# Optimization experiments

Measured on AMD Instinct MI355X. Metric: run time of the kernel, lower is better.

## Reference

```python
import jax, jax.numpy as jnp
import numpy as np

NUM_HEADS = 16
ROPE_BASE = 50.0


def _apply_rope(x):
    # x: [b, s, h, d]; torchtune-style rotary embedding with base=ROPE_BASE
    b, s, h, d = x.shape
    inv_freq = 1.0 / (ROPE_BASE ** (jnp.arange(0, d, 2, dtype=jnp.float32) / d))  # [d/2]
    angles = jnp.arange(s, dtype=jnp.float32)[:, None] * inv_freq[None, :]         # [s, d/2]
    cos = jnp.cos(angles)[None, :, None, :]  # [1, s, 1, d/2]
    sin = jnp.sin(angles)[None, :, None, :]
    xr = x.reshape(b, s, h, d // 2, 2)
    x0, x1 = xr[..., 0], xr[..., 1]
    out = jnp.stack([x0 * cos - x1 * sin, x1 * cos + x0 * sin], axis=-1)
    return out.reshape(b, s, h, d).astype(x.dtype)


def setup_inputs() -> dict:
    key = jax.random.key(0)
    k1, k2, k3 = jax.random.split(key, 3)
    B, S, D = 2, 2048, 1024
    x = jax.random.normal(k1, (B, S, D), dtype=jnp.float32)
    w_qkv = jax.random.normal(k2, (3 * D, D), dtype=jnp.float32) * (D ** -0.5)
    w_out = jax.random.normal(k3, (D, D), dtype=jnp.float32) * (D ** -0.5)
    b_out = jnp.zeros((D,), dtype=jnp.float32)
    return {"x": x, "w_qkv": w_qkv, "w_out": w_out, "b_out": b_out}


def reference(x, w_qkv, w_out, b_out):
    B, S, D = x.shape
    H = NUM_HEADS
    dk = D // H

    qkv = x @ w_qkv.T                       # [b, s, 3D]
    q, k, v = jnp.split(qkv, 3, axis=-1)
    q = q.reshape(B, S, H, dk)
    k = k.reshape(B, S, H, dk)
    q = _apply_rope(q)
    k = _apply_rope(k)
    q = q.transpose(0, 2, 1, 3)             # [b, h, s, d]
    k = k.transpose(0, 2, 1, 3)
    v = v.reshape(B, S, H, dk).transpose(0, 2, 1, 3)

    scale = 1.0 / jnp.sqrt(jnp.asarray(dk, dtype=x.dtype))
    scores = jnp.einsum('bhsd,bhtd->bhst', q, k) * scale  # [b, h, s, s]
    # additive diagonal mask: -inf on the diagonal (blocks self-attention)
    eye = jnp.eye(S, dtype=bool)
    scores = jnp.where(eye[None, None], -jnp.inf, scores)
    attn = jax.nn.softmax(scores, axis=-1)
    out = jnp.einsum('bhst,bhtd->bhsd', attn, v)          # [b, h, s, d]
    out = out.transpose(0, 2, 1, 3).reshape(B, S, D)
    return out @ w_out.T + b_out
```

## Files before the change

### kernel.cpp

```cpp
#include <hip/hip_runtime.h>
#include <hip/hip_bf16.h>
#include <math.h>
#include <type_traits>

#define D_MODEL 1024
#define NHEADS  16
#define DK      64
#define SEQ     2048
#define BATCH   2
#define QTILE   256

typedef __attribute__((ext_vector_type(8)))  short  short8;
typedef __attribute__((ext_vector_type(8)))  unsigned short ushort8;
typedef __attribute__((ext_vector_type(4)))  float  floatx4;
typedef __attribute__((ext_vector_type(16))) float  floatx16;

template <int N> using IC = std::integral_constant<int, N>;

__device__ __forceinline__ unsigned short f2bf(float f) {
    union { float f; unsigned int u; } v; v.f = f;
    unsigned int u = v.u;
    return (unsigned short)((u + 0x7FFFu + ((u >> 16) & 1u)) >> 16);
}
__device__ __forceinline__ float bf2f(unsigned short u) {
    union { unsigned int u; float f; } v; v.u = ((unsigned int)u) << 16;
    return v.f;
}
__device__ __forceinline__ unsigned int fau(float f) {
    union { float f; unsigned int u; } v; v.f = f; return v.u;
}

__device__ __forceinline__ void gload_lds16(const unsigned short* g, unsigned short* l) {
    __builtin_amdgcn_global_load_lds((__attribute__((address_space(1))) const void*)g,
                                     (__attribute__((address_space(3))) void*)l,
                                     16, 0, 0);
}

#define X8 ((BATCH * SEQ * D_MODEL) / 8)
#define W8 ((3 * D_MODEL * D_MODEL) / 8)
#define O8 ((D_MODEL * D_MODEL) / 8)
__global__ __launch_bounds__(256) void pack_all(const float* __restrict__ x,
                                                const float* __restrict__ wq,
                                                const float* __restrict__ wo,
                                                unsigned short* __restrict__ xb,
                                                unsigned short* __restrict__ wqb,
                                                unsigned short* __restrict__ wob) {
    const int t = blockIdx.x * blockDim.x + threadIdx.x;
    const float* src; unsigned short* dst; int idx;
    if (t < X8)           { src = x;  dst = xb;  idx = t; }
    else if (t < X8 + W8) { src = wq; dst = wqb; idx = t - X8; }
    else if (t < X8 + W8 + O8) { src = wo; dst = wob; idx = t - X8 - W8; }
    else return;
    const float4 a = ((const float4*)src)[2 * idx];
    const float4 b = ((const float4*)src)[2 * idx + 1];
    short8 o;
    o[0] = (short)f2bf(a.x); o[1] = (short)f2bf(a.y);
    o[2] = (short)f2bf(a.z); o[3] = (short)f2bf(a.w);
    o[4] = (short)f2bf(b.x); o[5] = (short)f2bf(b.y);
    o[6] = (short)f2bf(b.z); o[7] = (short)f2bf(b.w);
    ((short8*)dst)[idx] = o;
}

#define QKV_M 4096
#define QKV_N 3072
#define QKV_K 1024
#define QKV_NT (QKV_K / 64)

__global__ __launch_bounds__(512, 2) void gemm_qkv_8ph(const unsigned short* __restrict__ A,
                                                        const unsigned short* __restrict__ B,
                                                        unsigned short* __restrict__ C) {
    __shared__ __align__(16) unsigned short As[2][256][64];
    __shared__ __align__(16) unsigned short Bs[2][256][64];

    const int tid  = threadIdx.x;
    const int w    = tid >> 6;
    const int lane = tid & 63;
    const int quad = lane >> 4;
    const int lcol = lane & 15;
    const int wr   = w >> 2;
    const int wc   = w & 3;

    const int f  = blockIdx.x;
    const int wg = (f & 7) * 24 + (f >> 3);
    const int tn = (wg % (QKV_N / 256)) * 256;
    const int tm = (wg / (QKV_N / 256)) * 256;

    const int srow8 = lane >> 3;
    const int sj    = lane & 7;

    auto stageA = [&](int buf, int kt, int mh) {
#pragma unroll
        for (int c = 0; c < 2; ++c) {
            const int r0 = mh * 64 + c * 128 + w * 8;
            const int r  = r0 + srow8;
            gload_lds16(A + (size_t)(tm + r) * QKV_K + kt * 64 + ((sj ^ (r & 7)) * 8),
                        &As[buf][r0][0]);
        }
    };
    auto stageB = [&](int buf, int kt, int nh) {
#pragma unroll
        for (int c = 0; c < 2; ++c) {
            const int rho0 = c * 64 + w * 8;
            const int r0   = (rho0 >> 5) * 64 + nh * 32 + (rho0 & 31);
            const int r    = r0 + srow8;
            gload_lds16(B + (size_t)(tn + r) * QKV_K + kt * 64 + ((sj ^ (r & 7)) * 8),
                        &Bs[buf][r0][0]);
        }
    };

    floatx4 acc[8][4];
#pragma unroll
    for (int i = 0; i < 8; ++i)
#pragma unroll
        for (int j = 0; j < 4; ++j) acc[i][j] = (floatx4){0.f, 0.f, 0.f, 0.f};

    auto do_phase = [&](int buf, auto vmc, auto kkc, auto mhc, auto stager) {
        constexpr int VM = decltype(vmc)::value;
        constexpr int kk = decltype(kkc)::value;
        constexpr int mh = decltype(mhc)::value;
        if constexpr (VM == 2) asm volatile("s_waitcnt vmcnt(2)" ::: "memory");
        else                   asm volatile("s_waitcnt vmcnt(4)" ::: "memory");
        __builtin_amdgcn_s_barrier();
        asm volatile("" ::: "memory");
        short8 a[4], b[4];
#pragma unroll
        for (int i = 0; i < 4; ++i) {
            const int r = wr * 128 + mh * 64 + i * 16 + lcol;
            a[i] = *(const short8*)&As[buf][r][((kk * 4 + quad) ^ (r & 7)) * 8];
        }
#pragma unroll
        for (int j = 0; j < 4; ++j) {
            const int r = wc * 64 + j * 16 + lcol;
            b[j] = *(const short8*)&Bs[buf][r][((kk * 4 + quad) ^ (r & 7)) * 8];
        }
        stager();
        __builtin_amdgcn_s_setprio(1);
#pragma unroll
        for (int i = 0; i < 4; ++i)
#pragma unroll
            for (int j = 0; j < 4; ++j)
                acc[mh * 4 + i][j] = __builtin_amdgcn_mfma_f32_16x16x32_bf16(
                    a[i], b[j], acc[mh * 4 + i][j], 0, 0, 0);
        __builtin_amdgcn_s_setprio(0);
    };

    stageB(0, 0, 0); stageB(0, 0, 1); stageA(0, 0, 0); stageA(0, 0, 1);

    for (int t = 0; t < QKV_NT; ++t) {
        const int buf = t & 1, nb = buf ^ 1;
        const int kn = (t + 1 == QKV_NT) ? 0 : t + 1;
        do_phase(buf, IC<2>{}, IC<0>{}, IC<0>{}, [&] { stageB(nb, kn, 0); });
        do_phase(buf, IC<2>{}, IC<0>{}, IC<1>{}, [&] { stageB(nb, kn, 1); });
        do_phase(buf, IC<4>{}, IC<1>{}, IC<0>{}, [&] { stageA(nb, kn, 0); });
        do_phase(buf, IC<4>{}, IC<1>{}, IC<1>{}, [&] { stageA(nb, kn, 1); });
    }

#pragma unroll
    for (int i = 0; i < 8; ++i) {
#pragma unroll
        for (int rr = 0; rr < 4; ++rr) {
            const int row = tm + wr * 128 + i * 16 + quad * 4 + rr;
#pragma unroll
            for (int jf = 0; jf < 4; ++jf) {
                const int col = tn + wc * 64 + jf * 16 + lcol;
                C[(size_t)row * QKV_N + col] = f2bf(acc[i][jf][rr]);
            }
        }
    }
}

#define OUT_M 4096
#define OUT_N 1024
#define OUT_K 1024
#define OUT_NT (OUT_K / 64)

__global__ __launch_bounds__(512, 2) void gemm_out_8ph(const unsigned short* __restrict__ A,
                                                       const unsigned short* __restrict__ B,
                                                       const float* __restrict__ bias,
                                                       float* __restrict__ C) {
    __shared__ __align__(16) unsigned short As[2][128][64];
    __shared__ __align__(16) unsigned short Bs[2][128][64];

    const int tid  = threadIdx.x;
    const int w    = tid >> 6;
    const int lane = tid & 63;
    const int quad = lane >> 4;
    const int lcol = lane & 15;
    const int wr   = w >> 2;
    const int wc   = w & 3;

    const int f  = blockIdx.x;
    const int wg = (f & 7) * 32 + (f >> 3);
    const int tn = (wg & 7) * 128;
    const int tm = (wg >> 3) * 128;

    const int srow8 = lane >> 3;
    const int sj    = lane & 7;

    auto stageA = [&](int buf, int kt, int mh) {
        const int r0 = (w & 3) * 8 + mh * 32 + (w >> 2) * 64;
        const int r  = r0 + srow8;
        gload_lds16(A + (size_t)(tm + r) * OUT_K + kt * 64 + ((sj ^ (r & 7)) * 8),
                    &As[buf][r0][0]);
    };
    auto stageB = [&](int buf, int kt, int nh) {
        const int r0 = (w >> 1) * 32 + nh * 16 + (w & 1) * 8;
        const int r  = r0 + srow8;
        gload_lds16(B + (size_t)(tn + r) * OUT_K + kt * 64 + ((sj ^ (r & 7)) * 8),
                    &Bs[buf][r0][0]);
    };

    floatx4 acc[4][2];
#pragma unroll
    for (int i = 0; i < 4; ++i)
#pragma unroll
        for (int j = 0; j < 2; ++j) acc[i][j] = (floatx4){0.f, 0.f, 0.f, 0.f};

    auto do_phase = [&](int buf, auto vmc, auto kkc, auto mhc, auto stager) {
        constexpr int VM = decltype(vmc)::value;
        constexpr int kk = decltype(kkc)::value;
        constexpr int mh = decltype(mhc)::value;
        if constexpr (VM == 1) asm volatile("s_waitcnt vmcnt(1)" ::: "memory");
        else                   asm volatile("s_waitcnt vmcnt(2)" ::: "memory");
        __builtin_amdgcn_s_barrier();
        asm volatile("" ::: "memory");
        short8 a[2], b[2];
#pragma unroll
        for (int i = 0; i < 2; ++i) {
            const int r = wr * 64 + mh * 32 + i * 16 + lcol;
            a[i] = *(const short8*)&As[buf][r][((kk * 4 + quad) ^ (r & 7)) * 8];
        }
#pragma unroll
        for (int j = 0; j < 2; ++j) {
            const int r = wc * 32 + j * 16 + lcol;
            b[j] = *(const short8*)&Bs[buf][r][((kk * 4 + quad) ^ (r & 7)) * 8];
        }
        stager();
        __builtin_amdgcn_s_setprio(1);
#pragma unroll
        for (int i = 0; i < 2; ++i)
#pragma unroll
            for (int j = 0; j < 2; ++j)
                acc[mh * 2 + i][j] = __builtin_amdgcn_mfma_f32_16x16x32_bf16(
                    a[i], b[j], acc[mh * 2 + i][j], 0, 0, 0);
        __builtin_amdgcn_s_setprio(0);
    };

    stageB(0, 0, 0); stageB(0, 0, 1); stageA(0, 0, 0); stageA(0, 0, 1);

    for (int t = 0; t < OUT_NT; ++t) {
        const int buf = t & 1, nb = buf ^ 1;
        const int kn = (t + 1 == OUT_NT) ? 0 : t + 1;
        do_phase(buf, IC<1>{}, IC<0>{}, IC<0>{}, [&] { stageB(nb, kn, 0); });
        do_phase(buf, IC<1>{}, IC<0>{}, IC<1>{}, [&] { stageB(nb, kn, 1); });
        do_phase(buf, IC<2>{}, IC<1>{}, IC<0>{}, [&] { stageA(nb, kn, 0); });
        do_phase(buf, IC<2>{}, IC<1>{}, IC<1>{}, [&] { stageA(nb, kn, 1); });
    }

#pragma unroll
    for (int i = 0; i < 4; ++i) {
#pragma unroll
        for (int rr = 0; rr < 4; ++rr) {
            const int row = tm + wr * 64 + i * 16 + quad * 4 + rr;
#pragma unroll
            for (int j = 0; j < 2; ++j) {
                const int col = tn + wc * 32 + j * 16 + lcol;
                C[(size_t)row * OUT_N + col] = acc[i][j][rr] + bias[col];
            }
        }
    }
}

__global__ __launch_bounds__(256) void rope_vtrans(const unsigned short* __restrict__ qkvb,
                                                   unsigned short* __restrict__ Qb,
                                                   unsigned short* __restrict__ Kb,
                                                   unsigned short* __restrict__ Vtg) {
    const int st = blockIdx.x, h = blockIdx.y, b = blockIdx.z;
    const int tid = threadIdx.x;
    const int s0 = st * 64;

    const int i  = tid & 31;
    const int r0 = tid >> 5;
    const float inv_freq = exp2f(-(2.0f * (float)i / (float)DK) * log2f(50.0f));
    const float QSCALE = 0.125f * 1.44269504f;
#pragma unroll
    for (int pass = 0; pass < 8; ++pass) {
        const int s = s0 + r0 + pass * 8;
        const size_t in_base = ((size_t)(b * SEQ + s)) * (3 * D_MODEL) + h * DK + 2 * i;
        const float q0 = bf2f(qkvb[in_base]),           q1 = bf2f(qkvb[in_base + 1]);
        const float k0 = bf2f(qkvb[in_base + D_MODEL]), k1 = bf2f(qkvb[in_base + D_MODEL + 1]);
        float sn, cs;
        __sincosf((float)s * inv_freq, &sn, &cs);
        const size_t ob = (((size_t)(b * NHEADS + h)) * SEQ + s) * DK + 2 * i;
        const unsigned int qw = (unsigned int)f2bf((q0 * cs - q1 * sn) * QSCALE)
                              | ((unsigned int)f2bf((q1 * cs + q0 * sn) * QSCALE) << 16);
        const unsigned int kw = (unsigned int)f2bf(k0 * cs - k1 * sn)
                              | ((unsigned int)f2bf(k1 * cs + k0 * sn) << 16);
        *(unsigned int*)&Qb[ob] = qw;
        *(unsigned int*)&Kb[ob] = kw;
    }

    __shared__ unsigned short Lt[64][65];
    const int r = tid >> 3;
    const int c = (tid & 7) * 8;
    const size_t in_row = ((size_t)(b * SEQ + s0 + r)) * (3 * D_MODEL) + 2 * D_MODEL + h * DK + c;
    const ushort8 v0 = *(const ushort8*)&qkvb[in_row];
    const ushort8 v1 = *(const ushort8*)&qkvb[in_row + (size_t)32 * (3 * D_MODEL)];
    const int u0 = r, u1 = r + 32;
    const int kc0 = (u0 & 48) | (8 * ((u0 >> 2) & 1) + (u0 & 3) + 4 * ((u0 >> 3) & 1));
    const int kc1 = (u1 & 48) | (8 * ((u1 >> 2) & 1) + (u1 & 3) + 4 * ((u1 >> 3) & 1));
#pragma unroll
    for (int j = 0; j < 8; ++j) Lt[c + j][kc0] = v0[j];
#pragma unroll
    for (int j = 0; j < 8; ++j) Lt[c + j][kc1] = v1[j];
    __syncthreads();
    const size_t bh = (size_t)(b * NHEADS + h);
    ushort8 o0, o1;
#pragma unroll
    for (int j = 0; j < 8; ++j) { o0[j] = Lt[r][c + j]; o1[j] = Lt[r + 32][c + j]; }
    unsigned short* orow = Vtg + (bh * DK + r) * SEQ + s0 + c;
    *(ushort8*)orow = o0;
    *(ushort8*)(orow + (size_t)32 * SEQ) = o1;
}

#define LDW 72

__global__ __launch_bounds__(512, 2) void flash_attn(const unsigned short* __restrict__ Qb,
                                                     const unsigned short* __restrict__ Kb,
                                                     const unsigned short* __restrict__ Vtg,
                                                     unsigned short* __restrict__ attnb) {
    const int tid  = threadIdx.x;
    const int w8   = tid >> 6;
    const int lane = tid & 63;
    const int l31  = lane & 31;
    const int lh   = lane >> 5;

    const int f  = blockIdx.x + gridDim.x * (blockIdx.y + gridDim.y * blockIdx.z);
    const int w  = (f & 7) * 32 + (f >> 3);
    const int qt = w & 7;
    const int h  = (w >> 3) & 15;
    const int b  = w >> 7;

    __shared__ __align__(16) unsigned char smem[36864];
    unsigned short (*Ks0)[LDW] = (unsigned short (*)[LDW])(smem);
    unsigned short (*Vt0)[LDW] = (unsigned short (*)[LDW])(smem +  9216);
    unsigned short (*Ks1)[LDW] = (unsigned short (*)[LDW])(smem + 18432);
    unsigned short (*Vt1)[LDW] = (unsigned short (*)[LDW])(smem + 27648);

    const size_t bh = (size_t)(b * NHEADS + h);
    const unsigned short* Qg = Qb + (bh * SEQ + (size_t)qt * QTILE) * DK;
    const unsigned short* Kg = Kb + bh * SEQ * DK;
    const unsigned short* Vg = Vtg + bh * (size_t)DK * SEQ;

    short8 qf[4];
#pragma unroll
    for (int t = 0; t < 4; ++t)
        qf[t] = *(const short8*)&Qg[(size_t)(w8 * 32 + l31) * DK + t * 16 + lh * 8];

    const int strow = tid >> 3;
    const int stcol = (tid & 7) * 8;
    const unsigned short* kg = &Kg[(size_t)strow * DK + stcol];
    const unsigned short* vg = &Vg[(size_t)strow * SEQ + stcol];

    short8 kr = *(const short8*)&kg[0];
    short8 vr = *(const short8*)&vg[0];

    floatx16 oacc[2];
    oacc[0] = (floatx16)(0.f);
    oacc[1] = (floatx16)(0.f);
    float lp = 0.f;

    const int diagkt = qt * QTILE + (w8 >> 1) * 64;
    const int dH     = w8 & 1;

    auto compute = [&](unsigned short (*Ks)[LDW], unsigned short (*Vt)[LDW], int kt) {
        floatx16 sc0 = (floatx16)(0.f), sc1 = (floatx16)(0.f);
        __builtin_amdgcn_s_setprio(1);
#pragma unroll
        for (int t = 0; t < 4; ++t) {
            const short8 kf0 = *(short8*)&Ks[l31][t * 16 + lh * 8];
            const short8 kf1 = *(short8*)&Ks[32 + l31][t * 16 + lh * 8];
            sc0 = __builtin_amdgcn_mfma_f32_32x32x16_bf16(kf0, qf[t], sc0, 0, 0, 0);
            sc1 = __builtin_amdgcn_mfma_f32_32x32x16_bf16(kf1, qf[t], sc1, 0, 0, 0);
        }
        __builtin_amdgcn_s_setprio(0);

        if (kt == diagkt) {
#pragma unroll
            for (int r = 0; r < 16; ++r) {
                const int key_loc = (r & 3) + 8 * (r >> 2) + 4 * lh;
                if (key_loc == l31) { if (dH) sc1[r] = -1e30f; else sc0[r] = -1e30f; }
            }
        }

        short8 pf[4];
        {
            union { unsigned int u[4]; short8 s8; } g0, g1, g2, g3;
#pragma unroll
            for (int d = 0; d < 4; ++d) {
                const float a0 = __builtin_amdgcn_exp2f(sc0[2 * d]);
                const float a1 = __builtin_amdgcn_exp2f(sc0[2 * d + 1]);
                g0.u[d] = __builtin_amdgcn_perm(fau(a1), fau(a0), 0x07060302u);
                const float b0 = __builtin_amdgcn_exp2f(sc0[8 + 2 * d]);
                const float b1 = __builtin_amdgcn_exp2f(sc0[8 + 2 * d + 1]);
                g1.u[d] = __builtin_amdgcn_perm(fau(b1), fau(b0), 0x07060302u);
                const float c0 = __builtin_amdgcn_exp2f(sc1[2 * d]);
                const float c1 = __builtin_amdgcn_exp2f(sc1[2 * d + 1]);
                g2.u[d] = __builtin_amdgcn_perm(fau(c1), fau(c0), 0x07060302u);
                const float d0 = __builtin_amdgcn_exp2f(sc1[8 + 2 * d]);
                const float d1 = __builtin_amdgcn_exp2f(sc1[8 + 2 * d + 1]);
                g3.u[d] = __builtin_amdgcn_perm(fau(d1), fau(d0), 0x07060302u);
                lp += ((a0 + a1) + (b0 + b1)) + ((c0 + c1) + (d0 + d1));
            }
            pf[0] = g0.s8; pf[1] = g1.s8; pf[2] = g2.s8; pf[3] = g3.s8;
        }

        __builtin_amdgcn_s_setprio(1);
#pragma unroll
        for (int nd = 0; nd < 2; ++nd)
#pragma unroll
            for (int ks = 0; ks < 4; ++ks) {
                const short8 vf = *(short8*)&Vt[nd * 32 + l31][ks * 16 + lh * 8];
                oacc[nd] = __builtin_amdgcn_mfma_f32_32x32x16_bf16(pf[ks], vf, oacc[nd], 0, 0, 0);
            }
        __builtin_amdgcn_s_setprio(0);
    };

    for (int kt = 0; kt < SEQ; kt += 128) {
        *(short8*)&Ks0[strow][stcol] = kr;
        *(short8*)&Vt0[strow][stcol] = vr;
        __syncthreads();
        kr = *(const short8*)&kg[(size_t)(kt + 64) * DK];
        vr = *(const short8*)&vg[kt + 64];
        compute(Ks0, Vt0, kt);

        *(short8*)&Ks1[strow][stcol] = kr;
        *(short8*)&Vt1[strow][stcol] = vr;
        __syncthreads();
        const int ktn = (kt + 128 < SEQ) ? kt + 128 : 0;
        kr = *(const short8*)&kg[(size_t)ktn * DK];
        vr = *(const short8*)&vg[ktn];
        compute(Ks1, Vt1, kt + 64);
    }

    const float lptot = lp + __shfl_xor(lp, 32, 64);
    unsigned short* obase = attnb + ((size_t)b * SEQ + (size_t)qt * QTILE + w8 * 32) * D_MODEL
                          + h * DK;
#pragma unroll
    for (int r = 0; r < 16; ++r) {
        const int mq = (r & 3) + 8 * (r >> 2) + 4 * lh;
        const float inv = 1.001953125f / __shfl(lptot, mq, 64);
        obase[(size_t)mq * D_MODEL + l31]      = f2bf(oacc[0][r] * inv);
        obase[(size_t)mq * D_MODEL + 32 + l31] = f2bf(oacc[1][r] * inv);
    }
}

extern "C" void kernel_launch(void* const* d_in, const int* in_sizes, int n_in,
                              void* d_out, int out_size, void* d_ws, size_t ws_size,
                              hipStream_t stream) {
    const float* x     = (const float*)d_in[0];
    const float* w_qkv = (const float*)d_in[1];
    const float* w_out = (const float*)d_in[2];
    const float* b_out = (const float*)d_in[3];
    float* out = (float*)d_out;

    const int M = BATCH * SEQ;
    const size_t X_ELEMS    = (size_t)M * D_MODEL;
    const size_t WQKV_ELEMS = (size_t)3 * D_MODEL * D_MODEL;
    const size_t WOUT_ELEMS = (size_t)D_MODEL * D_MODEL;
    const size_t QKV_ELEMS  = (size_t)M * 3 * D_MODEL;
    const size_t HEAD_ELEMS = (size_t)BATCH * NHEADS * SEQ * DK;

    unsigned short* xb    = (unsigned short*)d_ws;
    unsigned short* wqkvb = xb + X_ELEMS;
    unsigned short* woutb = wqkvb + WQKV_ELEMS;
    unsigned short* qkvb  = woutb + WOUT_ELEMS;
    unsigned short* Qb    = qkvb + QKV_ELEMS;
    unsigned short* Kb    = Qb + HEAD_ELEMS;
    unsigned short* Vtg   = Kb + HEAD_ELEMS;
    unsigned short* attnb = Vtg + HEAD_ELEMS;

    pack_all<<<(X8 + W8 + O8 + 255) / 256, 256, 0, stream>>>(x, w_qkv, w_out, xb, wqkvb, woutb);

    gemm_qkv_8ph<<<(QKV_M / 256) * (QKV_N / 256), 512, 0, stream>>>(xb, wqkvb, qkvb);

    {
        dim3 grid(SEQ / 64, NHEADS, BATCH);
        rope_vtrans<<<grid, 256, 0, stream>>>(qkvb, Qb, Kb, Vtg);
    }
    {
        dim3 grid(SEQ / QTILE, NHEADS, BATCH);
        flash_attn<<<grid, 512, 0, stream>>>(Qb, Kb, Vtg, attnb);
    }
    gemm_out_8ph<<<(OUT_M / 128) * (OUT_N / 128), 512, 0, stream>>>(attnb, woutb, b_out, out);
}
```

Baseline: 182.8 us.

## Split key tiles across wave pairs with two query blocks per wave

Reorganizes the flash attention work split so each wave handles 64 query rows (two 32-row MFMA blocks) against half of each 64-key tile. The aim is to reuse each loaded K fragment for two score MFMAs and halve LDS reads of K per wave. Partial outputs and row sums from the two key-half waves are then combined through shared memory in a two-round epilogue before normalization. This adds extra syncs, an LDS reduction and more accumulator registers, which may hurt occupancy under the launch bounds.

```diff
diff --git a/kernel.cpp b/kernel.cpp
--- a/kernel.cpp
+++ b/kernel.cpp
@@ -330,10 +330,13 @@
                                                      const unsigned short* __restrict__ Vtg,
                                                      unsigned short* __restrict__ attnb) {
     const int tid  = threadIdx.x;
-    const int w8   = tid >> 6;
+    const int wv   = tid >> 6;
     const int lane = tid & 63;
     const int l31  = lane & 31;
     const int lh   = lane >> 5;
+    const int wq   = wv & 3;
+    const int kh   = wv >> 2;
+    const int kb   = kh * 32;
 
     const int f  = blockIdx.x + gridDim.x * (blockIdx.y + gridDim.y * blockIdx.z);
     const int w  = (f & 7) * 32 + (f >> 3);
@@ -346,16 +349,20 @@
     unsigned short (*Vt0)[LDW] = (unsigned short (*)[LDW])(smem +  9216);
     unsigned short (*Ks1)[LDW] = (unsigned short (*)[LDW])(smem + 18432);
     unsigned short (*Vt1)[LDW] = (unsigned short (*)[LDW])(smem + 27648);
+    float* Osh = (float*)smem;
+    float* lsh = (float*)(smem + 34816);
 
     const size_t bh = (size_t)(b * NHEADS + h);
     const unsigned short* Qg = Qb + (bh * SEQ + (size_t)qt * QTILE) * DK;
     const unsigned short* Kg = Kb + bh * SEQ * DK;
     const unsigned short* Vg = Vtg + bh * (size_t)DK * SEQ;
 
-    short8 qf[4];
-#pragma unroll
-    for (int t = 0; t < 4; ++t)
-        qf[t] = *(const short8*)&Qg[(size_t)(w8 * 32 + l31) * DK + t * 16 + lh * 8];
+    short8 qfA[4], qfB[4];
+#pragma unroll
+    for (int t = 0; t < 4; ++t) {
+        qfA[t] = *(const short8*)&Qg[(size_t)(wq * 64 + l31) * DK + t * 16 + lh * 8];
+        qfB[t] = *(const short8*)&Qg[(size_t)(wq * 64 + 32 + l31) * DK + t * 16 + lh * 8];
+    }
 
     const int strow = tid >> 3;
     const int stcol = (tid & 7) * 8;
@@ -365,64 +372,73 @@
     short8 kr = *(const short8*)&kg[0];
     short8 vr = *(const short8*)&vg[0];
 
-    floatx16 oacc[2];
-    oacc[0] = (floatx16)(0.f);
-    oacc[1] = (floatx16)(0.f);
-    float lp = 0.f;
-
-    const int diagkt = qt * QTILE + (w8 >> 1) * 64;
-    const int dH     = w8 & 1;
+    floatx16 oaccA[2], oaccB[2];
+    oaccA[0] = (floatx16)(0.f); oaccA[1] = (floatx16)(0.f);
+    oaccB[0] = (floatx16)(0.f); oaccB[1] = (floatx16)(0.f);
+    float lpA = 0.f, lpB = 0.f;
+
+    const int dktA = qt * QTILE + wq * 64 - kb;
+    const int dktB = dktA + 32;
 
     auto compute = [&](unsigned short (*Ks)[LDW], unsigned short (*Vt)[LDW], int kt) {
-        floatx16 sc0 = (floatx16)(0.f), sc1 = (floatx16)(0.f);
+        floatx16 scA = (floatx16)(0.f), scB = (floatx16)(0.f);
         __builtin_amdgcn_s_setprio(1);
 #pragma unroll
         for (int t = 0; t < 4; ++t) {
-            const short8 kf0 = *(short8*)&Ks[l31][t * 16 + lh * 8];
-            const short8 kf1 = *(short8*)&Ks[32 + l31][t * 16 + lh * 8];
-            sc0 = __builtin_amdgcn_mfma_f32_32x32x16_bf16(kf0, qf[t], sc0, 0, 0, 0);
-            sc1 = __builtin_amdgcn_mfma_f32_32x32x16_bf16(kf1, qf[t], sc1, 0, 0, 0);
+            const short8 kf = *(short8*)&Ks[kb + l31][t * 16 + lh * 8];
+            scA = __builtin_amdgcn_mfma_f32_32x32x16_bf16(kf, qfA[t], scA, 0, 0, 0);
+            scB = __builtin_amdgcn_mfma_f32_32x32x16_bf16(kf, qfB[t], scB, 0, 0, 0);
         }
         __builtin_amdgcn_s_setprio(0);
 
-        if (kt == diagkt) {
+        if (kt == dktA) {
 #pragma unroll
             for (int r = 0; r < 16; ++r) {
                 const int key_loc = (r & 3) + 8 * (r >> 2) + 4 * lh;
-                if (key_loc == l31) { if (dH) sc1[r] = -1e30f; else sc0[r] = -1e30f; }
-            }
-        }
-
-        short8 pf[4];
+                if (key_loc == l31) scA[r] = -1e30f;
+            }
+        }
+        if (kt == dktB) {
+#pragma unroll
+            for (int r = 0; r < 16; ++r) {
+                const int key_loc = (r & 3) + 8 * (r >> 2) + 4 * lh;
+                if (key_loc == l31) scB[r] = -1e30f;
+            }
+        }
+
+        short8 pA0, pA1, pB0, pB1;
         {
-            union { unsigned int u[4]; short8 s8; } g0, g1, g2, g3;
+            union { unsigned int u[4]; short8 s8; } a0, a1, b0, b1;
 #pragma unroll
             for (int d = 0; d < 4; ++d) {
-                const float a0 = __builtin_amdgcn_exp2f(sc0[2 * d]);
-                const float a1 = __builtin_amdgcn_exp2f(sc0[2 * d + 1]);
-                g0.u[d] = __builtin_amdgcn_perm(fau(a1), fau(a0), 0x07060302u);
-                const float b0 = __builtin_amdgcn_exp2f(sc0[8 + 2 * d]);
-                const float b1 = __builtin_amdgcn_exp2f(sc0[8 + 2 * d + 1]);
-                g1.u[d] = __builtin_amdgcn_perm(fau(b1), fau(b0), 0x07060302u);
-                const float c0 = __builtin_amdgcn_exp2f(sc1[2 * d]);
-                const float c1 = __builtin_amdgcn_exp2f(sc1[2 * d + 1]);
-                g2.u[d] = __builtin_amdgcn_perm(fau(c1), fau(c0), 0x07060302u);
-                const float d0 = __builtin_amdgcn_exp2f(sc1[8 + 2 * d]);
-                const float d1 = __builtin_amdgcn_exp2f(sc1[8 + 2 * d + 1]);
-                g3.u[d] = __builtin_amdgcn_perm(fau(d1), fau(d0), 0x07060302u);
-                lp += ((a0 + a1) + (b0 + b1)) + ((c0 + c1) + (d0 + d1));
-            }
-            pf[0] = g0.s8; pf[1] = g1.s8; pf[2] = g2.s8; pf[3] = g3.s8;
+                const float eA0 = __builtin_amdgcn_exp2f(scA[2 * d]);
+                const float eA1 = __builtin_amdgcn_exp2f(scA[2 * d + 1]);
+                a0.u[d] = __builtin_amdgcn_perm(fau(eA1), fau(eA0), 0x07060302u);
+                const float eA2 = __builtin_amdgcn_exp2f(scA[8 + 2 * d]);
+                const float eA3 = __builtin_amdgcn_exp2f(scA[8 + 2 * d + 1]);
+                a1.u[d] = __builtin_amdgcn_perm(fau(eA3), fau(eA2), 0x07060302u);
+                lpA += (eA0 + eA1) + (eA2 + eA3);
+                const float eB0 = __builtin_amdgcn_exp2f(scB[2 * d]);
+                const float eB1 = __builtin_amdgcn_exp2f(scB[2 * d + 1]);
+                b0.u[d] = __builtin_amdgcn_perm(fau(eB1), fau(eB0), 0x07060302u);
+                const float eB2 = __builtin_amdgcn_exp2f(scB[8 + 2 * d]);
+                const float eB3 = __builtin_amdgcn_exp2f(scB[8 + 2 * d + 1]);
+                b1.u[d] = __builtin_amdgcn_perm(fau(eB3), fau(eB2), 0x07060302u);
+                lpB += (eB0 + eB1) + (eB2 + eB3);
+            }
+            pA0 = a0.s8; pA1 = a1.s8; pB0 = b0.s8; pB1 = b1.s8;
         }
 
         __builtin_amdgcn_s_setprio(1);
 #pragma unroll
-        for (int nd = 0; nd < 2; ++nd)
-#pragma unroll
-            for (int ks = 0; ks < 4; ++ks) {
-                const short8 vf = *(short8*)&Vt[nd * 32 + l31][ks * 16 + lh * 8];
-                oacc[nd] = __builtin_amdgcn_mfma_f32_32x32x16_bf16(pf[ks], vf, oacc[nd], 0, 0, 0);
-            }
+        for (int nd = 0; nd < 2; ++nd) {
+            const short8 vf0 = *(short8*)&Vt[nd * 32 + l31][kb + lh * 8];
+            oaccA[nd] = __builtin_amdgcn_mfma_f32_32x32x16_bf16(pA0, vf0, oaccA[nd], 0, 0, 0);
+            oaccB[nd] = __builtin_amdgcn_mfma_f32_32x32x16_bf16(pB0, vf0, oaccB[nd], 0, 0, 0);
+            const short8 vf1 = *(short8*)&Vt[nd * 32 + l31][kb + 16 + lh * 8];
+            oaccA[nd] = __builtin_amdgcn_mfma_f32_32x32x16_bf16(pA1, vf1, oaccA[nd], 0, 0, 0);
+            oaccB[nd] = __builtin_amdgcn_mfma_f32_32x32x16_bf16(pB1, vf1, oaccB[nd], 0, 0, 0);
+        }
         __builtin_amdgcn_s_setprio(0);
     };
 
@@ -443,15 +459,47 @@
         compute(Ks1, Vt1, kt + 64);
     }
 
-    const float lptot = lp + __shfl_xor(lp, 32, 64);
-    unsigned short* obase = attnb + ((size_t)b * SEQ + (size_t)qt * QTILE + w8 * 32) * D_MODEL
+    const float ltA = lpA + __shfl_xor(lpA, 32, 64);
+    const float ltB = lpB + __shfl_xor(lpB, 32, 64);
+
+    __syncthreads();
+    if (kh == 1 && lh == 0) {
+        lsh[wq * 64 + l31]      = ltA;
+        lsh[wq * 64 + 32 + l31] = ltB;
+    }
+    unsigned short* obase = attnb + ((size_t)b * SEQ + (size_t)qt * QTILE + wq * 64) * D_MODEL
                           + h * DK;
-#pragma unroll
-    for (int r = 0; r < 16; ++r) {
-        const int mq = (r & 3) + 8 * (r >> 2) + 4 * lh;
-        const float inv = 1.001953125f / __shfl(lptot, mq, 64);
-        obase[(size_t)mq * D_MODEL + l31]      = f2bf(oacc[0][r] * inv);
-        obase[(size_t)mq * D_MODEL + 32 + l31] = f2bf(oacc[1][r] * inv);
+    for (int round = 0; round < 2; ++round) {
+        __syncthreads();
+        if (kh == 1 && (wq & 1) == round) {
+            const int base = (wq >> 1) * 64;
+#pragma unroll
+            for (int r = 0; r < 16; ++r) {
+                const int mq = (r & 3) + 8 * (r >> 2) + 4 * lh;
+                Osh[(base + mq) * 68 + l31]           = oaccA[0][r];
+                Osh[(base + mq) * 68 + 32 + l31]      = oaccA[1][r];
+                Osh[(base + 32 + mq) * 68 + l31]      = oaccB[0][r];
+                Osh[(base + 32 + mq) * 68 + 32 + l31] = oaccB[1][r];
+            }
+        }
+        __syncthreads();
+        if (kh == 0 && (wq & 1) == round) {
+            const int base = (wq >> 1) * 64;
+#pragma unroll
+            for (int r = 0; r < 16; ++r) {
+                const int mq = (r & 3) + 8 * (r >> 2) + 4 * lh;
+                const float invA = 1.001953125f / (__shfl(ltA, mq, 64) + lsh[wq * 64 + mq]);
+                const float invB = 1.001953125f / (__shfl(ltB, mq, 64) + lsh[wq * 64 + 32 + mq]);
+                const float vA0 = (oaccA[0][r] + Osh[(base + mq) * 68 + l31]) * invA;
+                const float vA1 = (oaccA[1][r] + Osh[(base + mq) * 68 + 32 + l31]) * invA;
+                const float vB0 = (oaccB[0][r] + Osh[(base + 32 + mq) * 68 + l31]) * invB;
+                const float vB1 = (oaccB[1][r] + Osh[(base + 32 + mq) * 68 + 32 + l31]) * invB;
+                obase[(size_t)mq * D_MODEL + l31]             = f2bf(vA0);
+                obase[(size_t)mq * D_MODEL + 32 + l31]        = f2bf(vA1);
+                obase[(size_t)(32 + mq) * D_MODEL + l31]      = f2bf(vB0);
+                obase[(size_t)(32 + mq) * D_MODEL + 32 + l31] = f2bf(vB1);
+            }
+        }
     }
 }
 
```

New measurement: 184.6 us. About the same (+0.9%).

## Use direct global-to-LDS loads with triple-buffered XOR-swizzled K/V tiles

Applied to the files above, without the earlier changes.

Replaces the register-staged, double-buffered K/V tile loads with direct global-to-LDS loads (gload_lds16) into a three-slot ring buffer. Padded LDS rows are replaced by an XOR swizzle to avoid bank conflicts. Each iteration now has a single barrier gated by s_waitcnt vmcnt(2), so loads run two tiles ahead of compute. LDS per block grows from 36 KB to 48 KB, which may affect occupancy. Correctness relies on the vmcnt accounting and the ring-slot reuse being race-free with only one barrier per step.

```diff
diff --git a/kernel.cpp b/kernel.cpp
--- a/kernel.cpp
+++ b/kernel.cpp
@@ -323,8 +323,6 @@
     *(ushort8*)(orow + (size_t)32 * SEQ) = o1;
 }
 
-#define LDW 72
-
 __global__ __launch_bounds__(512, 2) void flash_attn(const unsigned short* __restrict__ Qb,
                                                      const unsigned short* __restrict__ Kb,
                                                      const unsigned short* __restrict__ Vtg,
@@ -341,11 +339,7 @@
     const int h  = (w >> 3) & 15;
     const int b  = w >> 7;
 
-    __shared__ __align__(16) unsigned char smem[36864];
-    unsigned short (*Ks0)[LDW] = (unsigned short (*)[LDW])(smem);
-    unsigned short (*Vt0)[LDW] = (unsigned short (*)[LDW])(smem +  9216);
-    unsigned short (*Ks1)[LDW] = (unsigned short (*)[LDW])(smem + 18432);
-    unsigned short (*Vt1)[LDW] = (unsigned short (*)[LDW])(smem + 27648);
+    __shared__ __align__(16) unsigned char smem[49152];
 
     const size_t bh = (size_t)(b * NHEADS + h);
     const unsigned short* Qg = Qb + (bh * SEQ + (size_t)qt * QTILE) * DK;
@@ -357,13 +351,17 @@
     for (int t = 0; t < 4; ++t)
         qf[t] = *(const short8*)&Qg[(size_t)(w8 * 32 + l31) * DK + t * 16 + lh * 8];
 
-    const int strow = tid >> 3;
-    const int stcol = (tid & 7) * 8;
-    const unsigned short* kg = &Kg[(size_t)strow * DK + stcol];
-    const unsigned short* vg = &Vg[(size_t)strow * SEQ + stcol];
-
-    short8 kr = *(const short8*)&kg[0];
-    short8 vr = *(const short8*)&vg[0];
+    const int srow = tid >> 3;
+    const int swz  = ((tid & 7) ^ (srow & 7)) * 8;
+    const unsigned short* kgp = Kg + (size_t)srow * DK + swz;
+    const unsigned short* vgp = Vg + (size_t)srow * SEQ + swz;
+
+    auto stage = [&](int bufsel, int kt) {
+        unsigned short* Ks = (unsigned short*)(smem + bufsel * 16384);
+        unsigned short* Vt = Ks + 8192 / 2;
+        gload_lds16(kgp + (size_t)kt * DK, Ks + w8 * 512);
+        gload_lds16(vgp + kt,              Vt + w8 * 512);
+    };
 
     floatx16 oacc[2];
     oacc[0] = (floatx16)(0.f);
@@ -373,13 +371,18 @@
     const int diagkt = qt * QTILE + (w8 >> 1) * 64;
     const int dH     = w8 & 1;
 
-    auto compute = [&](unsigned short (*Ks)[LDW], unsigned short (*Vt)[LDW], int kt) {
+    auto compute = [&](int bufsel, int kt) {
+        const unsigned short* Ks = (const unsigned short*)(smem + bufsel * 16384);
+        const unsigned short* Vt = Ks + 8192 / 2;
+
         floatx16 sc0 = (floatx16)(0.f), sc1 = (floatx16)(0.f);
         __builtin_amdgcn_s_setprio(1);
 #pragma unroll
         for (int t = 0; t < 4; ++t) {
-            const short8 kf0 = *(short8*)&Ks[l31][t * 16 + lh * 8];
-            const short8 kf1 = *(short8*)&Ks[32 + l31][t * 16 + lh * 8];
+            const int c  = 2 * t + lh;
+            const int r0 = l31, r1 = 32 + l31;
+            const short8 kf0 = *(const short8*)&Ks[r0 * 64 + ((c ^ (r0 & 7)) * 8)];
+            const short8 kf1 = *(const short8*)&Ks[r1 * 64 + ((c ^ (r1 & 7)) * 8)];
             sc0 = __builtin_amdgcn_mfma_f32_32x32x16_bf16(kf0, qf[t], sc0, 0, 0, 0);
             sc1 = __builtin_amdgcn_mfma_f32_32x32x16_bf16(kf1, qf[t], sc1, 0, 0, 0);
         }
@@ -420,27 +423,27 @@
         for (int nd = 0; nd < 2; ++nd)
 #pragma unroll
             for (int ks = 0; ks < 4; ++ks) {
-                const short8 vf = *(short8*)&Vt[nd * 32 + l31][ks * 16 + lh * 8];
+                const int r = nd * 32 + l31;
+                const int c = 2 * ks + lh;
+                const short8 vf = *(const short8*)&Vt[r * 64 + ((c ^ (r & 7)) * 8)];
                 oacc[nd] = __builtin_amdgcn_mfma_f32_32x32x16_bf16(pf[ks], vf, oacc[nd], 0, 0, 0);
             }
         __builtin_amdgcn_s_setprio(0);
     };
 
-    for (int kt = 0; kt < SEQ; kt += 128) {
-        *(short8*)&Ks0[strow][stcol] = kr;
-        *(short8*)&Vt0[strow][stcol] = vr;
-        __syncthreads();
-        kr = *(const short8*)&kg[(size_t)(kt + 64) * DK];
-        vr = *(const short8*)&vg[kt + 64];
-        compute(Ks0, Vt0, kt);
-
-        *(short8*)&Ks1[strow][stcol] = kr;
-        *(short8*)&Vt1[strow][stcol] = vr;
-        __syncthreads();
-        const int ktn = (kt + 128 < SEQ) ? kt + 128 : 0;
-        kr = *(const short8*)&kg[(size_t)ktn * DK];
-        vr = *(const short8*)&vg[ktn];
-        compute(Ks1, Vt1, kt + 64);
+    stage(0, 0);
+    stage(1, 64);
+
+    int cur = 0;
+    for (int j = 0; j < 32; ++j) {
+        asm volatile("s_waitcnt vmcnt(2)" ::: "memory");
+        __builtin_amdgcn_s_barrier();
+        asm volatile("" ::: "memory");
+        const int nxt = (j + 2 < 32) ? j + 2 : j - 30;
+        const int nb  = (cur + 2 >= 3) ? cur - 1 : cur + 2;
+        stage(nb, nxt * 64);
+        compute(cur, j * 64);
+        cur = (cur == 2) ? 0 : cur + 1;
     }
 
     const float lptot = lp + __shfl_xor(lp, 32, 64);
```

Measured after the change: 187.5 us. 2.6% more time.
